# Kernel optimization log

Hardware: AMD Instinct MI355X
Metric: run time of the kernel (lower is better)

Reference implementation:

```python
import jax, jax.numpy as jnp
import numpy as np

M, K, N = 2048, 4096, 11008
Q_ABS_MAX = 128.0  # x_scaled_abs_max_fp for w8a8
Q_MIN, Q_MAX = -128, 127


def setup_inputs() -> dict:
    key = jax.random.key(0)
    k1, k2, k3, k4 = jax.random.split(key, 4)
    x = jax.random.normal(k1, (M, K), dtype=jnp.float32)
    # pre-quantized int8 weight, stored [K, N] (transposed layout as in quantize_weights)
    w_q = jax.random.randint(k2, (K, N), Q_MIN, Q_MAX + 1, dtype=jnp.int32).astype(jnp.int8)
    bias = jax.random.normal(k3, (N,), dtype=jnp.float32) * 0.01
    # per-tensor weight dequant scale (q_scale of the quantized weight)
    y_scale = jax.random.uniform(k4, (1,), dtype=jnp.float32, minval=0.001, maxval=0.02)
    return {"x": x, "w_q": w_q, "bias": bias, "y_scale": y_scale}


def reference(x, w_q, bias, y_scale):
    # dynamic per-tensor activation quantization: scale = max|x| / 128
    x_scale = jnp.max(jnp.abs(x)) / jnp.float32(Q_ABS_MAX)
    x_q = jnp.clip(jnp.round(x / x_scale), Q_MIN, Q_MAX).astype(jnp.int8)
    c = jnp.matmul(x_q.astype(jnp.int32), w_q.astype(jnp.int32))
    # dequantize + bias
    y = c.astype(jnp.float32) * (x_scale * y_scale[0]) + bias
    return y
```

## Files before the change

kernel.cpp:

```cpp
#include <hip/hip_runtime.h>
#include <stdint.h>

#define M_DIM 2048
#define K_DIM 4096
#define N_DIM 11008

typedef int v4i __attribute__((ext_vector_type(4)));

#define WS_XQ_OFF   65536ull
#define WS_WT_OFF   8454144ull
#define WS_FULL_BYTES (8454144ull + 45088768ull)
#define WS_SMALL_BYTES 8454144ull

static __device__ __forceinline__ void llds16(const void* g, void* l) {
  __builtin_amdgcn_global_load_lds(
      reinterpret_cast<const uint32_t __attribute__((address_space(1)))*>(
          reinterpret_cast<uintptr_t>(g)),
      reinterpret_cast<uint32_t __attribute__((address_space(3)))*>(
          reinterpret_cast<uintptr_t>(l)),
      16, 0, 0);
}

__global__ __launch_bounds__(256) void absmax_kernel(const float* __restrict__ x,
                                                     float* __restrict__ part) {
  __shared__ float red[256];
  const int g = blockIdx.x * 256 + threadIdx.x;
  const float4* x4 = reinterpret_cast<const float4*>(x);
  float m = 0.f;
#pragma unroll
  for (int i = 0; i < 8; ++i) {
    float4 v = x4[(size_t)i * 262144 + g];
    m = fmaxf(m, fmaxf(fmaxf(fabsf(v.x), fabsf(v.y)),
                       fmaxf(fabsf(v.z), fabsf(v.w))));
  }
  red[threadIdx.x] = m;
  __syncthreads();
  for (int s = 128; s > 0; s >>= 1) {
    if (threadIdx.x < s) red[threadIdx.x] = fmaxf(red[threadIdx.x], red[threadIdx.x + s]);
    __syncthreads();
  }
  if (threadIdx.x == 0) part[blockIdx.x] = red[0];
}

__global__ __launch_bounds__(256) void finalize_scale(const float* __restrict__ part,
                                                      const float* __restrict__ y_scale,
                                                      float* __restrict__ scales) {
  __shared__ float red[256];
  const int t = threadIdx.x;
  float m = fmaxf(fmaxf(part[t], part[t + 256]), fmaxf(part[t + 512], part[t + 768]));
  red[t] = m;
  __syncthreads();
  for (int s = 128; s > 0; s >>= 1) {
    if (t < s) red[t] = fmaxf(red[t], red[t + s]);
    __syncthreads();
  }
  if (t == 0) {
    float xs = red[0] * (1.0f / 128.0f);
    scales[0] = xs;
    scales[1] = xs * y_scale[0];
  }
}

__global__ __launch_bounds__(256) void quant_kernel(const float* __restrict__ x,
                                                    const float* __restrict__ scales,
                                                    signed char* __restrict__ xq) {
  const float s = scales[0];
  const size_t t = (size_t)blockIdx.x * 256 + threadIdx.x;
  const float4* x4 = reinterpret_cast<const float4*>(x) + t * 4;
  v4i o;
#pragma unroll
  for (int i = 0; i < 4; ++i) {
    float4 v = x4[i];
    int q0 = (int)rintf(v.x / s);
    int q1 = (int)rintf(v.y / s);
    int q2 = (int)rintf(v.z / s);
    int q3 = (int)rintf(v.w / s);
    q0 = max(-128, min(127, q0));
    q1 = max(-128, min(127, q1));
    q2 = max(-128, min(127, q2));
    q3 = max(-128, min(127, q3));
    o[i] = (q0 & 255) | ((q1 & 255) << 8) | ((q2 & 255) << 16) | ((q3 & 255) << 24);
  }
  *reinterpret_cast<v4i*>(xq + t * 16) = o;
}

__global__ __launch_bounds__(256) void transpose_pack(const int* __restrict__ w,
                                                      signed char* __restrict__ wt) {
  __shared__ int tile[64 * 65];
  const int t = threadIdx.x;
  const int n0 = blockIdx.x * 64;
  const int k0 = blockIdx.y * 64;
#pragma unroll
  for (int p = 0; p < 4; ++p) {
    const int id = p * 256 + t;
    const int r = id >> 4;
    const int c4 = id & 15;
    v4i v = *reinterpret_cast<const v4i*>(w + (size_t)(k0 + r) * N_DIM + n0 + c4 * 4);
    tile[r * 65 + c4 * 4 + 0] = v[0];
    tile[r * 65 + c4 * 4 + 1] = v[1];
    tile[r * 65 + c4 * 4 + 2] = v[2];
    tile[r * 65 + c4 * 4 + 3] = v[3];
  }
  __syncthreads();
  const int nl = t >> 2;
  const int kseg = t & 3;
  v4i o;
#pragma unroll
  for (int q = 0; q < 4; ++q) {
    const int kb = kseg * 16 + q * 4;
    int b0 = tile[(kb + 0) * 65 + nl] & 255;
    int b1 = tile[(kb + 1) * 65 + nl] & 255;
    int b2 = tile[(kb + 2) * 65 + nl] & 255;
    int b3 = tile[(kb + 3) * 65 + nl] & 255;
    o[q] = b0 | (b1 << 8) | (b2 << 16) | (b3 << 24);
  }
  *reinterpret_cast<v4i*>(wt + (size_t)(n0 + nl) * K_DIM + k0 + kseg * 16) = o;
}

#define TILE_B 24576
#define NT_K   (K_DIM / 64)

__global__ __launch_bounds__(256, 2) void gemm_i8_v2(
    const signed char* __restrict__ xq, const signed char* __restrict__ wt,
    const float* __restrict__ scales, const float* __restrict__ bias,
    float* __restrict__ y) {
  __shared__ __align__(16) signed char smem[3 * TILE_B];
  const int tid = threadIdx.x;

  const int bid = blockIdx.x;
  const int swz = (bid & 7) * 86 + (bid >> 3);
  const int m0 = (swz & 15) * 128;
  const int n0 = (swz >> 4) * 256;

  const int srow = tid >> 2;
  const int sseg = tid & 3;
  const int sgseg = sseg ^ ((srow ^ (srow >> 2)) & 3);
  const signed char* gA = xq + (size_t)(m0 + srow) * K_DIM + sgseg * 16;
  const signed char* gB = wt + (size_t)(n0 + srow) * K_DIM + sgseg * 16;
  signed char* const l0 = smem + tid * 16;

#define STAGE(kt, soff)                                                   \
  do {                                                                    \
    const size_t ko_ = (size_t)(kt) * 64;                                 \
    llds16(gA + ko_,                       l0 + (soff));                  \
    llds16(gA + ko_ + (size_t)64 * K_DIM,  l0 + (soff) + 4096);           \
    llds16(gB + ko_,                       l0 + (soff) + 8192);           \
    llds16(gB + ko_ + (size_t)64 * K_DIM,  l0 + (soff) + 12288);          \
    llds16(gB + ko_ + (size_t)128 * K_DIM, l0 + (soff) + 16384);          \
    llds16(gB + ko_ + (size_t)192 * K_DIM, l0 + (soff) + 20480);          \
  } while (0)

  const int lane = tid & 63;
  const int wid = tid >> 6;
  const int wm = wid >> 1;
  const int wn = wid & 1;
  const int l15 = lane & 15;
  const int kc = lane >> 4;
  const int rslot = (kc ^ ((l15 ^ (l15 >> 2)) & 3)) * 16;
  const int cA = (wm * 64 + l15) * 64 + rslot;
  const int cB = 8192 + (wn * 128 + l15) * 64 + rslot;

  v4i acc[4][8] = {};

#define COMPUTE(roff)                                                        \
  do {                                                                       \
    const signed char* bp_ = smem + (roff);                                  \
    v4i a_[4], b_[8];                                                        \
    _Pragma("unroll")                                                        \
    for (int m_ = 0; m_ < 4; ++m_)                                           \
      a_[m_] = *reinterpret_cast<const v4i*>(bp_ + cA + m_ * 1024);          \
    _Pragma("unroll")                                                        \
    for (int n_ = 0; n_ < 8; ++n_)                                           \
      b_[n_] = *reinterpret_cast<const v4i*>(bp_ + cB + n_ * 1024);          \
    _Pragma("unroll")                                                        \
    for (int m_ = 0; m_ < 4; ++m_)                                           \
      _Pragma("unroll")                                                      \
      for (int n_ = 0; n_ < 8; ++n_)                                         \
        acc[m_][n_] = __builtin_amdgcn_mfma_i32_16x16x64_i8(                 \
            a_[m_], b_[n_], acc[m_][n_], 0, 0, 0);                           \
  } while (0)

  STAGE(0, 0);
  STAGE(1, TILE_B);

  int rOff = 0;
  int sOff = 2 * TILE_B;
  for (int t = 0; t < NT_K - 2; ++t) {
    asm volatile("s_waitcnt vmcnt(6)" ::: "memory");
    __builtin_amdgcn_s_barrier();
    __builtin_amdgcn_sched_barrier(0);
    STAGE(t + 2, sOff);
    COMPUTE(rOff);
    rOff = (rOff == 2 * TILE_B) ? 0 : rOff + TILE_B;
    sOff = (sOff == 2 * TILE_B) ? 0 : sOff + TILE_B;
  }
  asm volatile("s_waitcnt vmcnt(6)" ::: "memory");
  __builtin_amdgcn_s_barrier();
  __builtin_amdgcn_sched_barrier(0);
  COMPUTE(rOff);
  rOff = (rOff == 2 * TILE_B) ? 0 : rOff + TILE_B;
  asm volatile("s_waitcnt vmcnt(0)" ::: "memory");
  __builtin_amdgcn_s_barrier();
  __builtin_amdgcn_sched_barrier(0);
  COMPUTE(rOff);

#undef STAGE
#undef COMPUTE

  const float s = scales[1];
#pragma unroll
  for (int n = 0; n < 8; ++n) {
    const int col = n0 + wn * 128 + n * 16 + l15;
    const float bv = bias[col];
#pragma unroll
    for (int m = 0; m < 4; ++m) {
      const int r0 = m0 + wm * 64 + m * 16 + kc * 4;
#pragma unroll
      for (int j = 0; j < 4; ++j)
        y[(size_t)(r0 + j) * N_DIM + col] = (float)acc[m][n][j] * s + bv;
    }
  }
}

#if defined(__has_builtin)
#if __has_builtin(__builtin_amdgcn_sdot4)
#define HAVE_SDOT4 1
#endif
#endif

static __device__ __forceinline__ int dot4(int a, int b, int c) {
#ifdef HAVE_SDOT4
  return __builtin_amdgcn_sdot4(a, b, c, false);
#else
  c += (int)(signed char)(a) * (int)(signed char)(b);
  c += (int)(signed char)(a >> 8) * (int)(signed char)(b >> 8);
  c += (int)(signed char)(a >> 16) * (int)(signed char)(b >> 16);
  c += (int)(signed char)(a >> 24) * (int)(signed char)(b >> 24);
  return c;
#endif
}

__global__ __launch_bounds__(256) void gemm_fallback(
    const signed char* __restrict__ xq, const int* __restrict__ w,
    const float* __restrict__ scales, const float* __restrict__ bias,
    float* __restrict__ y) {
  __shared__ int lds_a[64 * 17];
  __shared__ int lds_b[64 * 17];
  const int t = threadIdx.x;
  const int m0 = blockIdx.y * 64;
  const int n0 = blockIdx.x * 64;
  const int my = (t >> 4) * 4;
  const int nx = (t & 15) * 4;
  int acc[4][4] = {};
  for (int kt = 0; kt < K_DIM / 64; ++kt) {
    const int k0 = kt * 64;
    {
      const int r = t >> 2, sg = t & 3;
      v4i v = *reinterpret_cast<const v4i*>(xq + (size_t)(m0 + r) * K_DIM + k0 + sg * 16);
      lds_a[r * 17 + sg * 4 + 0] = v[0];
      lds_a[r * 17 + sg * 4 + 1] = v[1];
      lds_a[r * 17 + sg * 4 + 2] = v[2];
      lds_a[r * 17 + sg * 4 + 3] = v[3];
    }
    {
      const int n = t & 63, bkk = (t >> 6) * 4;
#pragma unroll
      for (int q = 0; q < 4; ++q) {
        const int kk = bkk + q;
        int b0 = w[(size_t)(k0 + kk * 4 + 0) * N_DIM + n0 + n] & 255;
        int b1 = w[(size_t)(k0 + kk * 4 + 1) * N_DIM + n0 + n] & 255;
        int b2 = w[(size_t)(k0 + kk * 4 + 2) * N_DIM + n0 + n] & 255;
        int b3 = w[(size_t)(k0 + kk * 4 + 3) * N_DIM + n0 + n] & 255;
        lds_b[n * 17 + kk] = b0 | (b1 << 8) | (b2 << 16) | (b3 << 24);
      }
    }
    __syncthreads();
#pragma unroll
    for (int kk = 0; kk < 16; ++kk) {
      int a[4], b[4];
#pragma unroll
      for (int i = 0; i < 4; ++i) a[i] = lds_a[(my + i) * 17 + kk];
#pragma unroll
      for (int j = 0; j < 4; ++j) b[j] = lds_b[(nx + j) * 17 + kk];
#pragma unroll
      for (int i = 0; i < 4; ++i)
#pragma unroll
        for (int j = 0; j < 4; ++j) acc[i][j] = dot4(a[i], b[j], acc[i][j]);
    }
    __syncthreads();
  }
  const float s = scales[1];
#pragma unroll
  for (int i = 0; i < 4; ++i)
#pragma unroll
    for (int j = 0; j < 4; ++j)
      y[(size_t)(m0 + my + i) * N_DIM + n0 + nx + j] =
          (float)acc[i][j] * s + bias[n0 + nx + j];
}

extern "C" void kernel_launch(void* const* d_in, const int* in_sizes, int n_in,
                              void* d_out, int out_size, void* d_ws, size_t ws_size,
                              hipStream_t stream) {
  (void)in_sizes; (void)n_in; (void)out_size;
  const float* x = (const float*)d_in[0];
  const int* w = (const int*)d_in[1];
  const float* bias = (const float*)d_in[2];
  const float* yscale = (const float*)d_in[3];
  float* y = (float*)d_out;
  char* ws = (char*)d_ws;
  float* scales = (float*)(ws);
  float* part = (float*)(ws + 1024);
  signed char* xq = (signed char*)(ws + WS_XQ_OFF);
  signed char* wt = (signed char*)(ws + WS_WT_OFF);

  if (ws_size < WS_SMALL_BYTES) return;

  absmax_kernel<<<1024, 256, 0, stream>>>(x, part);
  finalize_scale<<<1, 256, 0, stream>>>(part, yscale, scales);
  quant_kernel<<<2048, 256, 0, stream>>>(x, scales, xq);
  if (ws_size >= WS_FULL_BYTES) {
    transpose_pack<<<dim3(N_DIM / 64, K_DIM / 64), 256, 0, stream>>>(w, wt);
    gemm_i8_v2<<<(M_DIM / 128) * (N_DIM / 256), 256, 0, stream>>>(xq, wt, scales, bias, y);
  } else {
    gemm_fallback<<<dim3(N_DIM / 64, M_DIM / 64), 256, 0, stream>>>(xq, w, scales, bias, y);
  }
}
```

Baseline: 172.4 us.

## Restructure int8 GEMM into 8-wave ping-pong with BK=128 and split staging

Replaces the 4-wave, BK=64 GEMM with an 8-wave (512-thread) kernel. Each wave now computes a 64x64 sub-tile, and K tiles are 128 bytes with a new 8-segment XOR swizzle. Each K tile is split into two compute phases interleaved with half-stage global-to-LDS loads. Barriers and s_setprio raise MFMA issue priority so one wave group computes while the other loads. The aim is better overlap of LDS reads, global loads and MFMA work. In exchange, LDS use per block roughly doubles, so two blocks per CU may no longer fit, and there are more barriers per tile.

```diff
diff --git a/kernel.cpp b/kernel.cpp
--- a/kernel.cpp
+++ b/kernel.cpp
@@ -117,14 +117,17 @@
   *reinterpret_cast<v4i*>(wt + (size_t)(n0 + nl) * K_DIM + k0 + kseg * 16) = o;
 }
 
-#define TILE_B 24576
-#define NT_K   (K_DIM / 64)
-
-__global__ __launch_bounds__(256, 2) void gemm_i8_v2(
+#define BKB     128
+#define A_BYTES (128 * BKB)
+#define B_BYTES (256 * BKB)
+#define TILE3_B (A_BYTES + B_BYTES)
+#define NT3     (K_DIM / BKB)
+
+__global__ __launch_bounds__(512, 2) void gemm_i8_v3(
     const signed char* __restrict__ xq, const signed char* __restrict__ wt,
     const float* __restrict__ scales, const float* __restrict__ bias,
     float* __restrict__ y) {
-  __shared__ __align__(16) signed char smem[3 * TILE_B];
+  __shared__ __align__(16) signed char smem[3 * TILE3_B];
   const int tid = threadIdx.x;
 
   const int bid = blockIdx.x;
@@ -132,85 +135,102 @@
   const int m0 = (swz & 15) * 128;
   const int n0 = (swz >> 4) * 256;
 
-  const int srow = tid >> 2;
-  const int sseg = tid & 3;
-  const int sgseg = sseg ^ ((srow ^ (srow >> 2)) & 3);
-  const signed char* gA = xq + (size_t)(m0 + srow) * K_DIM + sgseg * 16;
-  const signed char* gB = wt + (size_t)(n0 + srow) * K_DIM + sgseg * 16;
-  signed char* const l0 = smem + tid * 16;
-
-#define STAGE(kt, soff)                                                   \
+  const int srow = tid >> 3;
+  const int sseg = tid & 7;
+  const int sgoff = (sseg ^ (srow & 7)) * 16;
+  const signed char* gA = xq + (size_t)(m0 + srow) * K_DIM + sgoff;
+  const signed char* gB = wt + (size_t)(n0 + srow) * K_DIM + sgoff;
+  signed char* const ld = smem + tid * 16;
+
+#define STAGE_P0(kt, soff)                                                \
   do {                                                                    \
-    const size_t ko_ = (size_t)(kt) * 64;                                 \
-    llds16(gA + ko_,                       l0 + (soff));                  \
-    llds16(gA + ko_ + (size_t)64 * K_DIM,  l0 + (soff) + 4096);           \
-    llds16(gB + ko_,                       l0 + (soff) + 8192);           \
-    llds16(gB + ko_ + (size_t)64 * K_DIM,  l0 + (soff) + 12288);          \
-    llds16(gB + ko_ + (size_t)128 * K_DIM, l0 + (soff) + 16384);          \
-    llds16(gB + ko_ + (size_t)192 * K_DIM, l0 + (soff) + 20480);          \
+    const size_t ko_ = (size_t)(kt) * BKB;                                \
+    llds16(gA + ko_,                      ld + (soff));                   \
+    llds16(gA + ko_ + (size_t)64 * K_DIM, ld + (soff) + 8192);            \
+    llds16(gB + ko_,                      ld + (soff) + A_BYTES);         \
+  } while (0)
+#define STAGE_P1(kt, soff)                                                \
+  do {                                                                    \
+    const size_t ko_ = (size_t)(kt) * BKB;                                \
+    llds16(gB + ko_ + (size_t)64  * K_DIM, ld + (soff) + A_BYTES + 8192); \
+    llds16(gB + ko_ + (size_t)128 * K_DIM, ld + (soff) + A_BYTES + 16384);\
+    llds16(gB + ko_ + (size_t)192 * K_DIM, ld + (soff) + A_BYTES + 24576);\
   } while (0)
 
   const int lane = tid & 63;
   const int wid = tid >> 6;
-  const int wm = wid >> 1;
-  const int wn = wid & 1;
+  const int wm = wid >> 2;
+  const int wn = wid & 3;
   const int l15 = lane & 15;
   const int kc = lane >> 4;
-  const int rslot = (kc ^ ((l15 ^ (l15 >> 2)) & 3)) * 16;
-  const int cA = (wm * 64 + l15) * 64 + rslot;
-  const int cB = 8192 + (wn * 128 + l15) * 64 + rslot;
-
-  v4i acc[4][8] = {};
-
-#define COMPUTE(roff)                                                        \
+  const int sx0 = ((0 + kc) ^ (l15 & 7)) * 16;
+  const int sx1 = ((4 + kc) ^ (l15 & 7)) * 16;
+  const int offA = (wm * 64 + l15) * BKB;
+  const int offB = A_BYTES + (wn * 64 + l15) * BKB;
+
+  v4i acc[4][4] = {};
+
+#define CPHASE(roff, sx)                                                     \
   do {                                                                       \
     const signed char* bp_ = smem + (roff);                                  \
-    v4i a_[4], b_[8];                                                        \
+    v4i a_[4], b_[4];                                                        \
     _Pragma("unroll")                                                        \
     for (int m_ = 0; m_ < 4; ++m_)                                           \
-      a_[m_] = *reinterpret_cast<const v4i*>(bp_ + cA + m_ * 1024);          \
+      a_[m_] = *reinterpret_cast<const v4i*>(bp_ + offA + m_ * 2048 + (sx)); \
     _Pragma("unroll")                                                        \
-    for (int n_ = 0; n_ < 8; ++n_)                                           \
-      b_[n_] = *reinterpret_cast<const v4i*>(bp_ + cB + n_ * 1024);          \
+    for (int n_ = 0; n_ < 4; ++n_)                                           \
+      b_[n_] = *reinterpret_cast<const v4i*>(bp_ + offB + n_ * 2048 + (sx)); \
+    __builtin_amdgcn_s_barrier();                                            \
+    asm volatile("s_waitcnt lgkmcnt(0)" ::: "memory");                       \
+    __builtin_amdgcn_sched_barrier(0);                                       \
+    __builtin_amdgcn_s_setprio(1);                                           \
     _Pragma("unroll")                                                        \
     for (int m_ = 0; m_ < 4; ++m_)                                           \
       _Pragma("unroll")                                                      \
-      for (int n_ = 0; n_ < 8; ++n_)                                         \
+      for (int n_ = 0; n_ < 4; ++n_)                                         \
         acc[m_][n_] = __builtin_amdgcn_mfma_i32_16x16x64_i8(                 \
             a_[m_], b_[n_], acc[m_][n_], 0, 0, 0);                           \
+    __builtin_amdgcn_s_setprio(0);                                           \
   } while (0)
 
-  STAGE(0, 0);
-  STAGE(1, TILE_B);
+  STAGE_P0(0, 0);
+  STAGE_P1(0, 0);
+  STAGE_P0(1, TILE3_B);
+  STAGE_P1(1, TILE3_B);
+  asm volatile("s_waitcnt vmcnt(6)" ::: "memory");
+  __builtin_amdgcn_s_barrier();
 
   int rOff = 0;
-  int sOff = 2 * TILE_B;
-  for (int t = 0; t < NT_K - 2; ++t) {
+  int sOff = 2 * TILE3_B;
+  for (int t = 0; t < NT3 - 2; ++t) {
+    STAGE_P0(t + 2, sOff);
+    CPHASE(rOff, sx0);
+    __builtin_amdgcn_s_barrier();
+    STAGE_P1(t + 2, sOff);
+    CPHASE(rOff, sx1);
     asm volatile("s_waitcnt vmcnt(6)" ::: "memory");
     __builtin_amdgcn_s_barrier();
-    __builtin_amdgcn_sched_barrier(0);
-    STAGE(t + 2, sOff);
-    COMPUTE(rOff);
-    rOff = (rOff == 2 * TILE_B) ? 0 : rOff + TILE_B;
-    sOff = (sOff == 2 * TILE_B) ? 0 : sOff + TILE_B;
-  }
-  asm volatile("s_waitcnt vmcnt(6)" ::: "memory");
+    rOff = (rOff == 2 * TILE3_B) ? 0 : rOff + TILE3_B;
+    sOff = (sOff == 2 * TILE3_B) ? 0 : sOff + TILE3_B;
+  }
+  CPHASE(rOff, sx0);
   __builtin_amdgcn_s_barrier();
-  __builtin_amdgcn_sched_barrier(0);
-  COMPUTE(rOff);
-  rOff = (rOff == 2 * TILE_B) ? 0 : rOff + TILE_B;
+  CPHASE(rOff, sx1);
   asm volatile("s_waitcnt vmcnt(0)" ::: "memory");
   __builtin_amdgcn_s_barrier();
-  __builtin_amdgcn_sched_barrier(0);
-  COMPUTE(rOff);
-
-#undef STAGE
-#undef COMPUTE
+  rOff = (rOff == 2 * TILE3_B) ? 0 : rOff + TILE3_B;
+  CPHASE(rOff, sx0);
+  __builtin_amdgcn_s_barrier();
+  CPHASE(rOff, sx1);
+
+#undef STAGE_P0
+#undef STAGE_P1
+#undef CPHASE
 
   const float s = scales[1];
 #pragma unroll
-  for (int n = 0; n < 8; ++n) {
-    const int col = n0 + wn * 128 + n * 16 + l15;
+  for (int n = 0; n < 4; ++n) {
+    const int col = n0 + wn * 64 + n * 16 + l15;
     const float bv = bias[col];
 #pragma unroll
     for (int m = 0; m < 4; ++m) {
@@ -320,7 +340,7 @@
   quant_kernel<<<2048, 256, 0, stream>>>(x, scales, xq);
   if (ws_size >= WS_FULL_BYTES) {
     transpose_pack<<<dim3(N_DIM / 64, K_DIM / 64), 256, 0, stream>>>(w, wt);
-    gemm_i8_v2<<<(M_DIM / 128) * (N_DIM / 256), 256, 0, stream>>>(xq, wt, scales, bias, y);
+    gemm_i8_v3<<<(M_DIM / 128) * (N_DIM / 256), 512, 0, stream>>>(xq, wt, scales, bias, y);
   } else {
     gemm_fallback<<<dim3(N_DIM / 64, M_DIM / 64), 256, 0, stream>>>(xq, w, scales, bias, y);
   }
```

New measurement: 173.9 us. About the same (+0.9%).

## Use 512-thread GEMM blocks with 8 waves and smaller per-wave tiles

Applied to the files above, without the earlier changes.

Splits the 128x256 GEMM tile across 8 waves (2x4) instead of 4, giving each wave a 64x64 sub-tile with half the accumulators. Each thread issues 3 LDS-direct loads per stage instead of 6. The LDS swizzle pattern changes, and the wait/barrier now comes after the compute so one barrier per iteration both guards reuse and signals readiness. This aims to raise wave occupancy and latency hiding with less register pressure, at the cost of more LDS reads per MFMA (lower operand reuse per wave).

```diff
diff --git a/kernel.cpp b/kernel.cpp
--- a/kernel.cpp
+++ b/kernel.cpp
@@ -117,14 +117,14 @@
   *reinterpret_cast<v4i*>(wt + (size_t)(n0 + nl) * K_DIM + k0 + kseg * 16) = o;
 }
 
-#define TILE_B 24576
-#define NT_K   (K_DIM / 64)
-
-__global__ __launch_bounds__(256, 2) void gemm_i8_v2(
+#define V4_TILE_B 24576
+#define V4_NT     (K_DIM / 64)
+
+__global__ __launch_bounds__(512, 4) void gemm_i8_v4(
     const signed char* __restrict__ xq, const signed char* __restrict__ wt,
     const float* __restrict__ scales, const float* __restrict__ bias,
     float* __restrict__ y) {
-  __shared__ __align__(16) signed char smem[3 * TILE_B];
+  __shared__ __align__(16) signed char smem[3 * V4_TILE_B];
   const int tid = threadIdx.x;
 
   const int bid = blockIdx.x;
@@ -134,74 +134,71 @@
 
   const int srow = tid >> 2;
   const int sseg = tid & 3;
-  const int sgseg = sseg ^ ((srow ^ (srow >> 2)) & 3);
-  const signed char* gA = xq + (size_t)(m0 + srow) * K_DIM + sgseg * 16;
-  const signed char* gB = wt + (size_t)(n0 + srow) * K_DIM + sgseg * 16;
-  signed char* const l0 = smem + tid * 16;
-
-#define STAGE(kt, soff)                                                   \
-  do {                                                                    \
-    const size_t ko_ = (size_t)(kt) * 64;                                 \
-    llds16(gA + ko_,                       l0 + (soff));                  \
-    llds16(gA + ko_ + (size_t)64 * K_DIM,  l0 + (soff) + 4096);           \
-    llds16(gB + ko_,                       l0 + (soff) + 8192);           \
-    llds16(gB + ko_ + (size_t)64 * K_DIM,  l0 + (soff) + 12288);          \
-    llds16(gB + ko_ + (size_t)128 * K_DIM, l0 + (soff) + 16384);          \
-    llds16(gB + ko_ + (size_t)192 * K_DIM, l0 + (soff) + 20480);          \
+  const int sgoff = (sseg ^ ((srow >> 1) & 3)) * 16;
+  const signed char* gA  = xq + (size_t)(m0 + srow) * K_DIM + sgoff;
+  const signed char* gB0 = wt + (size_t)(n0 + srow) * K_DIM + sgoff;
+  const signed char* gB1 = wt + (size_t)(n0 + 128 + srow) * K_DIM + sgoff;
+  signed char* const ldA  = smem + tid * 16;
+  signed char* const ldB0 = smem + 8192 + tid * 16;
+  signed char* const ldB1 = smem + 16384 + tid * 16;
+
+#define STAGE(kt, soff)                                   \
+  do {                                                    \
+    const size_t ko_ = (size_t)(kt) * 64;                 \
+    llds16(gA + ko_,  ldA + (soff));                      \
+    llds16(gB0 + ko_, ldB0 + (soff));                     \
+    llds16(gB1 + ko_, ldB1 + (soff));                     \
   } while (0)
 
   const int lane = tid & 63;
   const int wid = tid >> 6;
-  const int wm = wid >> 1;
-  const int wn = wid & 1;
+  const int wm = wid >> 2;
+  const int wn = wid & 3;
   const int l15 = lane & 15;
   const int kc = lane >> 4;
-  const int rslot = (kc ^ ((l15 ^ (l15 >> 2)) & 3)) * 16;
-  const int cA = (wm * 64 + l15) * 64 + rslot;
-  const int cB = 8192 + (wn * 128 + l15) * 64 + rslot;
-
-  v4i acc[4][8] = {};
+  const int segoff = (kc ^ ((l15 >> 1) & 3)) * 16;
+  const int offA = (wm * 64 + l15) * 64 + segoff;
+  const int offB = 8192 + (wn * 64 + l15) * 64 + segoff;
+
+  v4i acc[4][4] = {};
 
 #define COMPUTE(roff)                                                        \
   do {                                                                       \
     const signed char* bp_ = smem + (roff);                                  \
-    v4i a_[4], b_[8];                                                        \
+    v4i a_[4], b_[4];                                                        \
     _Pragma("unroll")                                                        \
     for (int m_ = 0; m_ < 4; ++m_)                                           \
-      a_[m_] = *reinterpret_cast<const v4i*>(bp_ + cA + m_ * 1024);          \
+      a_[m_] = *reinterpret_cast<const v4i*>(bp_ + offA + m_ * 1024);        \
     _Pragma("unroll")                                                        \
-    for (int n_ = 0; n_ < 8; ++n_)                                           \
-      b_[n_] = *reinterpret_cast<const v4i*>(bp_ + cB + n_ * 1024);          \
+    for (int n_ = 0; n_ < 4; ++n_)                                           \
+      b_[n_] = *reinterpret_cast<const v4i*>(bp_ + offB + n_ * 1024);        \
     _Pragma("unroll")                                                        \
     for (int m_ = 0; m_ < 4; ++m_)                                           \
       _Pragma("unroll")                                                      \
-      for (int n_ = 0; n_ < 8; ++n_)                                         \
+      for (int n_ = 0; n_ < 4; ++n_)                                         \
         acc[m_][n_] = __builtin_amdgcn_mfma_i32_16x16x64_i8(                 \
             a_[m_], b_[n_], acc[m_][n_], 0, 0, 0);                           \
   } while (0)
 
   STAGE(0, 0);
-  STAGE(1, TILE_B);
+  STAGE(1, V4_TILE_B);
+  asm volatile("s_waitcnt vmcnt(3)" ::: "memory");
+  __builtin_amdgcn_s_barrier();
 
   int rOff = 0;
-  int sOff = 2 * TILE_B;
-  for (int t = 0; t < NT_K - 2; ++t) {
-    asm volatile("s_waitcnt vmcnt(6)" ::: "memory");
-    __builtin_amdgcn_s_barrier();
-    __builtin_amdgcn_sched_barrier(0);
+  int sOff = 2 * V4_TILE_B;
+  for (int t = 0; t < V4_NT - 2; ++t) {
     STAGE(t + 2, sOff);
     COMPUTE(rOff);
-    rOff = (rOff == 2 * TILE_B) ? 0 : rOff + TILE_B;
-    sOff = (sOff == 2 * TILE_B) ? 0 : sOff + TILE_B;
-  }
-  asm volatile("s_waitcnt vmcnt(6)" ::: "memory");
-  __builtin_amdgcn_s_barrier();
-  __builtin_amdgcn_sched_barrier(0);
+    asm volatile("s_waitcnt vmcnt(3)" ::: "memory");
+    __builtin_amdgcn_s_barrier();
+    rOff = (rOff == 2 * V4_TILE_B) ? 0 : rOff + V4_TILE_B;
+    sOff = (sOff == 2 * V4_TILE_B) ? 0 : sOff + V4_TILE_B;
+  }
   COMPUTE(rOff);
-  rOff = (rOff == 2 * TILE_B) ? 0 : rOff + TILE_B;
   asm volatile("s_waitcnt vmcnt(0)" ::: "memory");
   __builtin_amdgcn_s_barrier();
-  __builtin_amdgcn_sched_barrier(0);
+  rOff = (rOff == 2 * V4_TILE_B) ? 0 : rOff + V4_TILE_B;
   COMPUTE(rOff);
 
 #undef STAGE
@@ -209,8 +206,8 @@
 
   const float s = scales[1];
 #pragma unroll
-  for (int n = 0; n < 8; ++n) {
-    const int col = n0 + wn * 128 + n * 16 + l15;
+  for (int n = 0; n < 4; ++n) {
+    const int col = n0 + wn * 64 + n * 16 + l15;
     const float bv = bias[col];
 #pragma unroll
     for (int m = 0; m < 4; ++m) {
@@ -320,7 +317,7 @@
   quant_kernel<<<2048, 256, 0, stream>>>(x, scales, xq);
   if (ws_size >= WS_FULL_BYTES) {
     transpose_pack<<<dim3(N_DIM / 64, K_DIM / 64), 256, 0, stream>>>(w, wt);
-    gemm_i8_v2<<<(M_DIM / 128) * (N_DIM / 256), 256, 0, stream>>>(xq, wt, scales, bias, y);
+    gemm_i8_v4<<<(M_DIM / 128) * (N_DIM / 256), 512, 0, stream>>>(xq, wt, scales, bias, y);
   } else {
     gemm_fallback<<<dim3(N_DIM / 64, M_DIM / 64), 256, 0, stream>>>(xq, w, scales, bias, y);
   }
```

Measured after the change: 169.3 us. No clear change (-1.8%).
